# Kernel tuning notes

Hardware: AMD Instinct MI355X
Metric: run time of the kernel (lower is better)

The kernel has to match this reference:

```python
import jax, jax.numpy as jnp
import numpy as np

UNITS = 512
MODELS = 64
BATCH = 64
INPUT_DIM = 512


def setup_inputs() -> dict:
    key = jax.random.key(0)
    ks = jax.random.split(key, 6)
    scale = 0.05  # keep gates in a sane range like 'random_normal' init
    return {
        "inputs": jax.random.normal(ks[0], (MODELS, BATCH, INPUT_DIM), jnp.float32),
        "h_tm1": jax.random.normal(ks[1], (MODELS, BATCH, UNITS), jnp.float32),
        "c_tm1": jax.random.normal(ks[2], (MODELS, BATCH, UNITS), jnp.float32),
        "kernel": jax.random.normal(ks[3], (MODELS, INPUT_DIM, 4 * UNITS), jnp.float32) * scale,
        "recurrent_kernel": jax.random.normal(ks[4], (MODELS, UNITS, 4 * UNITS), jnp.float32) * scale,
        "bias": jax.random.normal(ks[5], (MODELS, 1, 4 * UNITS), jnp.float32) * scale,
    }


def reference(inputs, h_tm1, c_tm1, kernel, recurrent_kernel, bias):
    # batched over the models axis: [m,b,d] @ [m,d,4u] -> [m,b,4u]
    z = jnp.einsum('mbd,mdu->mbu', inputs, kernel)
    z = z + jnp.einsum('mbh,mhu->mbu', h_tm1, recurrent_kernel)
    z = z + bias  # broadcasts over batch
    z0, z1, z2, z3 = jnp.split(z, 4, axis=-1)
    i = jax.nn.sigmoid(z0)
    f = jax.nn.sigmoid(z1)
    c = f * c_tm1 + i * jnp.tanh(z2)
    o = jax.nn.sigmoid(z3)
    h = o * jnp.tanh(c)
    return (h, h, c)
```

## Files before the change

### kernel.cpp

```cpp
#include <hip/hip_runtime.h>
#include <hip/hip_bf16.h>

#define MODELS 64
#define BATCH 64
#define IN_DIM 512
#define UNITS 512
#define NCOLS 2048
#define GRAN_PER_TENSOR (MODELS * 16 * 4 * 64)

typedef __attribute__((ext_vector_type(8))) short short8;
typedef __attribute__((ext_vector_type(4))) float f32x4;

static __device__ __forceinline__ short f2bf(float f) {
    return __builtin_bit_cast(short, __float2bfloat16(f));
}
static __device__ __forceinline__ float sigmoidf_(float x) {
    return 1.0f / (1.0f + __expf(-x));
}
static __device__ __forceinline__ float tanhf_(float x) {
    float e = __expf(-2.0f * fabsf(x));
    float r = (1.0f - e) / (1.0f + e);
    return copysignf(r, x);
}

__global__ __launch_bounds__(256) void prepack_A_kernel(
    const float* __restrict__ x, const float* __restrict__ h,
    short8* __restrict__ P)
{
    const int t = blockIdx.x * 256 + threadIdx.x;
    const int tensor = t >> 18;
    const int r = t & (GRAN_PER_TENSOR - 1);
    const int kg = r & 3;
    const int row = (r >> 2) & 63;
    const int ks = (r >> 8) & 15;
    const int m = r >> 12;
    const float* src = (tensor ? h : x) + ((size_t)(m * 64 + row) * 512 + ks * 32 + kg * 8);
    f32x4 a0 = *(const f32x4*)src;
    f32x4 a1 = *(const f32x4*)(src + 4);
    short8 v;
    v[0] = f2bf(a0[0]); v[1] = f2bf(a0[1]); v[2] = f2bf(a0[2]); v[3] = f2bf(a0[3]);
    v[4] = f2bf(a1[0]); v[5] = f2bf(a1[1]); v[6] = f2bf(a1[2]); v[7] = f2bf(a1[3]);
    P[(size_t)tensor * GRAN_PER_TENSOR + (size_t)((m * 16 + ks) * 4 + kg) * 64 + row] = v;
}

__global__ __launch_bounds__(256, 2) void lstm_main_kernel(
    const float* __restrict__ c_tm1,
    const float* __restrict__ kernel_,
    const float* __restrict__ rkernel,
    const float* __restrict__ bias,
    const short8* __restrict__ Pa,
    float* __restrict__ out)
{
    __shared__ float lds[16384];

    const int bid = blockIdx.x;
    const int m = bid >> 3;
    const int u0 = (bid & 7) * 64;

    const int tid = threadIdx.x;
    const int w = tid >> 6;
    const int lane = tid & 63;
    const int col16 = lane & 15;
    const int kq = lane >> 4;
    const int ucol = u0 + w * 16 + col16;

    const float* wbase[2] = { kernel_ + (size_t)m * IN_DIM * NCOLS,
                              rkernel + (size_t)m * UNITS * NCOLS };
    const short8* pabase[2] = { Pa + (size_t)m * 4096,
                                Pa + GRAN_PER_TENSOR + (size_t)m * 4096 };

    int soff[8];
#pragma unroll
    for (int j = 0; j < 8; ++j) {
        const int row = j * 4 + w;
        const int q = lane ^ ((((row >> 3) & 1)) << 2);
        const int g = q >> 4;
        const int cq = q & 15;
        soff[j] = row * NCOLS + g * 512 + u0 + cq * 4;
    }

    f32x4 acc[4][4];
#pragma unroll
    for (int bt = 0; bt < 4; ++bt)
#pragma unroll
        for (int g = 0; g < 4; ++g) acc[bt][g] = (f32x4){0.f, 0.f, 0.f, 0.f};

    auto STAGE = [&](int step, int bufsel) {
        const float* wb = wbase[step >> 4] + (size_t)(step & 15) * 32 * NCOLS;
#pragma unroll
        for (int j = 0; j < 8; ++j) {
            const float* src = wb + soff[j];
            float* dst = lds + bufsel * 8192 + j * 1024 + w * 256;
            __builtin_amdgcn_global_load_lds(
                (const __attribute__((address_space(1))) void*)src,
                (__attribute__((address_space(3))) void*)dst, 16, 0, 0);
        }
    };
    auto LOADA = [&](int step, short8 (&af)[4]) {
        const short8* pb = pabase[step >> 4] + (size_t)((step & 15) * 4 + kq) * 64 + col16;
#pragma unroll
        for (int bt = 0; bt < 4; ++bt)
            asm volatile("global_load_dwordx4 %0, %1, off"
                         : "=v"(af[bt]) : "v"(pb + bt * 16) : "memory");
    };
    auto COMPUTE = [&](int bufsel, short8 (&af)[4]) {
        const float* lb = lds + bufsel * 8192 + kq * 8 * 256;
        const int cb = w * 16 + col16;
#pragma unroll
        for (int g = 0; g < 4; ++g) {
            const int rd = (g * 64 + cb) ^ ((kq & 1) << 4);
            short8 bfr;
#pragma unroll
            for (int i = 0; i < 8; ++i) bfr[i] = f2bf(lb[rd + i * 256]);
#pragma unroll
            for (int bt = 0; bt < 4; ++bt)
                acc[bt][g] = __builtin_amdgcn_mfma_f32_16x16x32_bf16(
                    af[bt], bfr, acc[bt][g], 0, 0, 0);
        }
    };

#define WAITV(N, af)                                                         \
    asm volatile("s_waitcnt vmcnt(" #N ")"                                   \
                 : "+v"(af[0]), "+v"(af[1]), "+v"(af[2]), "+v"(af[3])        \
                 :: "memory")
#define BAR() asm volatile("s_barrier" ::: "memory")
#define LGKM0() asm volatile("s_waitcnt lgkmcnt(0)" ::: "memory")

    short8 afA[4], afB[4];
    STAGE(0, 0);
    LOADA(0, afA);

    for (int sp = 0; sp < 16; ++sp) {
        const int te = 2 * sp;
        STAGE(te + 1, 1);
        LOADA(te + 1, afB);
        WAITV(12, afA); BAR();
        COMPUTE(0, afA);
        LGKM0(); BAR();
        if (sp < 15) {
            STAGE(te + 2, 0);
            LOADA(te + 2, afA);
            WAITV(12, afB);
        } else {
            WAITV(0, afB);
        }
        BAR();
        COMPUTE(1, afB);
        LGKM0(); BAR();
    }

    const float* bp = bias + (size_t)m * NCOLS;
    const float bi = bp[0 * 512 + ucol];
    const float bff = bp[1 * 512 + ucol];
    const float bcc = bp[2 * 512 + ucol];
    const float bo = bp[3 * 512 + ucol];

    const size_t mbase = (size_t)m * (BATCH * UNITS);
    const float* cprev = c_tm1 + mbase;
    float* hout0 = out;
    float* hout1 = out + (size_t)MODELS * BATCH * UNITS;
    float* cout = out + 2 * (size_t)MODELS * BATCH * UNITS;

#pragma unroll
    for (int bt = 0; bt < 4; ++bt) {
#pragma unroll
        for (int r = 0; r < 4; ++r) {
            const int b = bt * 16 + kq * 4 + r;
            const float z0 = acc[bt][0][r] + bi;
            const float z1 = acc[bt][1][r] + bff;
            const float z2 = acc[bt][2][r] + bcc;
            const float z3 = acc[bt][3][r] + bo;
            const float ig = sigmoidf_(z0);
            const float fg = sigmoidf_(z1);
            const float cand = tanhf_(z2);
            const float og = sigmoidf_(z3);
            const size_t idx = (size_t)b * UNITS + ucol;
            const float c = fg * cprev[idx] + ig * cand;
            const float hh = og * tanhf_(c);
            hout0[mbase + idx] = hh;
            hout1[mbase + idx] = hh;
            cout[mbase + idx] = c;
        }
    }
}

extern "C" void kernel_launch(void* const* d_in, const int* in_sizes, int n_in,
                              void* d_out, int out_size, void* d_ws, size_t ws_size,
                              hipStream_t stream) {
    const float* inputs = (const float*)d_in[0];
    const float* h_tm1 = (const float*)d_in[1];
    const float* c_tm1 = (const float*)d_in[2];
    const float* kernel_ = (const float*)d_in[3];
    const float* rkernel = (const float*)d_in[4];
    const float* bias = (const float*)d_in[5];
    float* out = (float*)d_out;

    short8* P = (short8*)d_ws;
    hipLaunchKernelGGL(prepack_A_kernel, dim3(2 * GRAN_PER_TENSOR / 256), dim3(256),
                       0, stream, inputs, h_tm1, P);
    hipLaunchKernelGGL(lstm_main_kernel, dim3(MODELS * 8), dim3(256), 0, stream,
                       c_tm1, kernel_, rkernel, bias, P, out);
}
```

Measured before the change: 134.9 us.

## Give each wave a private LDS slice to drop workgroup barriers

Each wave now stages into its own LDS region only the weight columns it consumes. The staging offsets and the swizzled read indices are rearranged to match. With no cross-wave sharing of LDS, the s_barrier calls are replaced by per-wave lgkmcnt waits and scheduling barriers, removing the stalls where waves wait on each other. In exchange, correctness now rests on each wave's own waitcnt ordering of the async global-to-LDS loads, and the new swizzle may change LDS bank-conflict behaviour.

```diff
diff --git a/kernel.cpp b/kernel.cpp
--- a/kernel.cpp
+++ b/kernel.cpp
@@ -43,7 +43,7 @@
     P[(size_t)tensor * GRAN_PER_TENSOR + (size_t)((m * 16 + ks) * 4 + kg) * 64 + row] = v;
 }
 
-__global__ __launch_bounds__(256, 2) void lstm_main_kernel(
+__global__ __launch_bounds__(256, 2) void lstm_nobar_kernel(
     const float* __restrict__ c_tm1,
     const float* __restrict__ kernel_,
     const float* __restrict__ rkernel,
@@ -64,6 +64,8 @@
     const int kq = lane >> 4;
     const int ucol = u0 + w * 16 + col16;
 
+    float* wlds = lds + w * 4096;
+
     const float* wbase[2] = { kernel_ + (size_t)m * IN_DIM * NCOLS,
                               rkernel + (size_t)m * UNITS * NCOLS };
     const short8* pabase[2] = { Pa + (size_t)m * 4096,
@@ -72,11 +74,9 @@
     int soff[8];
 #pragma unroll
     for (int j = 0; j < 8; ++j) {
-        const int row = j * 4 + w;
-        const int q = lane ^ ((((row >> 3) & 1)) << 2);
-        const int g = q >> 4;
-        const int cq = q & 15;
-        soff[j] = row * NCOLS + g * 512 + u0 + cq * 4;
+        const int q = lane ^ ((j & 2) << 1);
+        const int rr = q >> 4, g = (q >> 2) & 3, p = q & 3;
+        soff[j] = (j * 4 + rr) * NCOLS + g * 512 + u0 + w * 16 + p * 4;
     }
 
     f32x4 acc[4][4];
@@ -90,7 +90,7 @@
 #pragma unroll
         for (int j = 0; j < 8; ++j) {
             const float* src = wb + soff[j];
-            float* dst = lds + bufsel * 8192 + j * 1024 + w * 256;
+            float* dst = wlds + bufsel * 2048 + j * 256;
             __builtin_amdgcn_global_load_lds(
                 (const __attribute__((address_space(1))) void*)src,
                 (__attribute__((address_space(3))) void*)dst, 16, 0, 0);
@@ -104,14 +104,17 @@
                          : "=v"(af[bt]) : "v"(pb + bt * 16) : "memory");
     };
     auto COMPUTE = [&](int bufsel, short8 (&af)[4]) {
-        const float* lb = lds + bufsel * 8192 + kq * 8 * 256;
-        const int cb = w * 16 + col16;
+        const float* lb = wlds + bufsel * 2048;
 #pragma unroll
         for (int g = 0; g < 4; ++g) {
-            const int rd = (g * 64 + cb) ^ ((kq & 1) << 4);
             short8 bfr;
 #pragma unroll
-            for (int i = 0; i < 8; ++i) bfr[i] = f2bf(lb[rd + i * 256]);
+            for (int i = 0; i < 8; ++i) {
+                const int kr = kq * 8 + i;
+                const int j = kr >> 2, rr = kr & 3;
+                const int slot = ((rr << 4) | (g << 2) | (col16 >> 2)) ^ ((j & 2) << 1);
+                bfr[i] = f2bf(lb[j * 256 + slot * 4 + (col16 & 3)]);
+            }
 #pragma unroll
             for (int bt = 0; bt < 4; ++bt)
                 acc[bt][g] = __builtin_amdgcn_mfma_f32_16x16x32_bf16(
@@ -123,8 +126,8 @@
     asm volatile("s_waitcnt vmcnt(" #N ")"                                   \
                  : "+v"(af[0]), "+v"(af[1]), "+v"(af[2]), "+v"(af[3])        \
                  :: "memory")
-#define BAR() asm volatile("s_barrier" ::: "memory")
 #define LGKM0() asm volatile("s_waitcnt lgkmcnt(0)" ::: "memory")
+#define SB0() __builtin_amdgcn_sched_barrier(0)
 
     short8 afA[4], afB[4];
     STAGE(0, 0);
@@ -132,21 +135,22 @@
 
     for (int sp = 0; sp < 16; ++sp) {
         const int te = 2 * sp;
+        LGKM0();
         STAGE(te + 1, 1);
         LOADA(te + 1, afB);
-        WAITV(12, afA); BAR();
+        WAITV(12, afA);
+        SB0();
         COMPUTE(0, afA);
-        LGKM0(); BAR();
         if (sp < 15) {
+            LGKM0();
             STAGE(te + 2, 0);
             LOADA(te + 2, afA);
             WAITV(12, afB);
         } else {
             WAITV(0, afB);
         }
-        BAR();
+        SB0();
         COMPUTE(1, afB);
-        LGKM0(); BAR();
     }
 
     const float* bp = bias + (size_t)m * NCOLS;
@@ -198,6 +202,6 @@
     short8* P = (short8*)d_ws;
     hipLaunchKernelGGL(prepack_A_kernel, dim3(2 * GRAN_PER_TENSOR / 256), dim3(256),
                        0, stream, inputs, h_tm1, P);
-    hipLaunchKernelGGL(lstm_main_kernel, dim3(MODELS * 8), dim3(256), 0, stream,
+    hipLaunchKernelGGL(lstm_nobar_kernel, dim3(MODELS * 8), dim3(256), 0, stream,
                        c_tm1, kernel_, rkernel, bias, P, out);
 }
```

New measurement: 157.2 us. 1.17x slower.
